# Performance work log

Hardware: AMD Instinct MI355X
Metric: run time of the kernel (lower is better)

Reference implementation:

```python
import jax, jax.numpy as jnp
import numpy as np
from jax import lax

K = 512          # num_embeddings
D = 64           # embedding_dim
BETA = 0.25      # commitment_cost


def _conv(x, w, b, stride, pad):
    y = lax.conv_general_dilated(x, w, (stride, stride), ((pad, pad), (pad, pad)),
                                 dimension_numbers=('NCHW', 'OIHW', 'NCHW'))
    return y + b[None, :, None, None]


def _convT(x, w, b, stride, k, pad):
    # transposed conv as lhs-dilated conv; w is OIHW with O=out_channels
    p = k - 1 - pad
    y = lax.conv_general_dilated(x, w, (1, 1), ((p, p), (p, p)),
                                 lhs_dilation=(stride, stride),
                                 dimension_numbers=('NCHW', 'OIHW', 'NCHW'))
    return y + b[None, :, None, None]


def setup_inputs() -> dict:
    key = jax.random.key(0)
    ks = jax.random.split(key, 16)
    s = 0.05
    inp = {
        'x':   jax.random.uniform(ks[0], (16, 3, 256, 256), jnp.float32),
        'w1':  jax.random.normal(ks[1], (128, 3, 4, 4), jnp.float32) * s,
        'b1':  jnp.zeros((128,), jnp.float32),
        'w2':  jax.random.normal(ks[2], (256, 128, 4, 4), jnp.float32) * s,
        'b2':  jnp.zeros((256,), jnp.float32),
        'w3':  jax.random.normal(ks[3], (D, 256, 3, 3), jnp.float32) * s,
        'b3':  jnp.zeros((D,), jnp.float32),
        'emb': jax.random.uniform(ks[4], (K, D), jnp.float32, -1.0 / K, 1.0 / K),
        'wt1': jax.random.normal(ks[5], (256, D, 4, 4), jnp.float32) * s,
        'bt1': jnp.zeros((256,), jnp.float32),
        'wt2': jax.random.normal(ks[6], (128, 256, 4, 4), jnp.float32) * s,
        'bt2': jnp.zeros((128,), jnp.float32),
        'w4':  jax.random.normal(ks[7], (3, 128, 3, 3), jnp.float32) * s,
        'b4':  jnp.zeros((3,), jnp.float32),
    }
    return inp


def reference(x, w1, b1, w2, b2, w3, b3, emb, wt1, bt1, wt2, bt2, w4, b4):
    # ---- encoder ----
    h = jax.nn.relu(_conv(x, w1, b1, 2, 1))    # [B,128,128,128]
    h = jax.nn.relu(_conv(h, w2, b2, 2, 1))    # [B,256,64,64]
    z = _conv(h, w3, b3, 1, 1)                 # [B,64,64,64]

    # ---- vector quantizer (faithful raw-memory reshape, as in source) ----
    flat_z = z.reshape(-1, D)                                 # [N,D]
    dists = (jnp.sum(flat_z ** 2, axis=1, keepdims=True)
             + jnp.sum(emb ** 2, axis=1)
             - 2.0 * flat_z @ emb.T)                          # [N,K]
    idx = jnp.argmin(dists, axis=1)                           # [N]
    quantized = emb[idx].reshape(z.shape)                     # gather == onehot @ emb

    e_latent = jnp.mean((lax.stop_gradient(quantized) - z) ** 2)
    q_latent = jnp.mean((quantized - lax.stop_gradient(z)) ** 2)
    vq_loss = q_latent + BETA * e_latent

    z_q = z + lax.stop_gradient(quantized - z)                # straight-through

    n = flat_z.shape[0]
    avg_probs = jnp.zeros((K,), jnp.float32).at[idx].add(1.0) / n
    perplexity = jnp.exp(-jnp.sum(avg_probs * jnp.log(avg_probs + 1e-10)))

    # ---- decoder (computed in the original forward; its output is unused) ----
    d = jax.nn.relu(_convT(z_q, wt1, bt1, 2, 4, 1))           # [B,256,128,128]
    d = jax.nn.relu(_convT(d, wt2, bt2, 2, 4, 1))             # [B,128,256,256]
    _x_recon = jax.nn.sigmoid(_conv(d, w4, b4, 1, 1))         # [B,3,256,256]

    return (z_q, vq_loss, perplexity)
```

## Files before the change

### kernel.cpp

```cpp
#include <hip/hip_runtime.h>
#include <math.h>

typedef __attribute__((ext_vector_type(8))) short bf16x8;
typedef __attribute__((ext_vector_type(4))) float f32x4;
typedef __attribute__((ext_vector_type(4))) unsigned u32x4;
typedef __attribute__((ext_vector_type(2))) unsigned u32x2;

#define H1P_OFF  0ull
#define H2P_OFF  35143680ull
#define WQ2H_OFF 53526528ull
#define WQ2L_OFF 53788672ull
#define WQ3H_OFF 54050816ull
#define WQ3L_OFF 54149120ull
#define EQ_OFF   54247424ull
#define EN_OFF   54280192ull
#define HIST_OFF 54280704ull
#define SSEP_OFF 54284800ull
#define WQ1H_OFF 54285824ull
#define WQ1L_OFF 54289920ull

__device__ inline unsigned short f2bf(float f) {
  unsigned u = __builtin_bit_cast(unsigned, f);
  return (unsigned short)((u + 0x7fffu + ((u >> 16) & 1u)) >> 16);
}
__device__ inline float bf2f(unsigned short h) {
  return __builtin_bit_cast(float, (unsigned)h << 16);
}
__device__ inline unsigned packsplit(float v) {
  unsigned short h = f2bf(v);
  unsigned short l = f2bf(v - bf2f(h));
  return (unsigned)h | ((unsigned)l << 16);
}
#define SEL_HI 0x05040100u
#define SEL_LO 0x07060302u
__device__ inline bf16x8 mkfrag(const u32x4 p, const u32x4 q, unsigned sel) {
  u32x4 r;
  r[0] = __builtin_amdgcn_perm(p[1], p[0], sel);
  r[1] = __builtin_amdgcn_perm(p[3], p[2], sel);
  r[2] = __builtin_amdgcn_perm(q[1], q[0], sel);
  r[3] = __builtin_amdgcn_perm(q[3], q[2], sel);
  return __builtin_bit_cast(bf16x8, r);
}

__global__ void pack_wq1_k(const float* __restrict__ w, unsigned short* __restrict__ wh) {
  int i = blockIdx.x * 256 + threadIdx.x;
  if (i >= 8192) return;
  int j = i & 7, l = (i >> 3) & 63, fg = (i >> 9) & 7, ks = i >> 12;
  int row = fg * 16 + (l & 15);
  int k = ks * 32 + (l >> 4) * 8 + j;
  int ci = k >> 4, r = k & 15, kh = r >> 2, kw = r & 3;
  wh[i] = (ci < 3) ? f2bf(w[((row * 3 + ci) * 4 + kh) * 4 + kw]) : (unsigned short)0;
}
__global__ void pack_wq2_k(const float* __restrict__ w, unsigned short* __restrict__ wh) {
  int i = blockIdx.x * 256 + threadIdx.x;
  if (i >= 524288) return;
  int j = i & 7, l = (i >> 3) & 63, fg = (i >> 9) & 15, ks = i >> 13;
  int row = fg * 16 + (l & 15);
  int k = ks * 32 + (l >> 4) * 8 + j;
  wh[i] = f2bf(w[row * 2048 + k]);
}
__global__ void pack_wq3_k(const float* __restrict__ w, unsigned short* __restrict__ wh) {
  int i = blockIdx.x * 256 + threadIdx.x;
  if (i >= 196608) return;
  int j = i & 7, l = (i >> 3) & 63, fg = (i >> 9) & 3, ks = i >> 11;
  int row = fg * 16 + (l & 15);
  int k = ks * 32 + (l >> 4) * 8 + j;
  int ci = k / 12, rb = k - ci * 12, kh = rb >> 2, kw = rb & 3;
  wh[i] = (kw < 3) ? f2bf(w[((row * 256 + ci) * 3 + kh) * 3 + kw]) : (unsigned short)0;
}
__global__ void pack_eq_k(const float* __restrict__ emb, unsigned* __restrict__ eq,
                          float* __restrict__ enorm) {
  int i = blockIdx.x * 256 + threadIdx.x;
  if (i < 32768) {
    int e = i & 3, l = (i >> 2) & 63, j = (i >> 8) & 1, fg = (i >> 9) & 31, ks = i >> 14;
    int row = fg * 16 + (l & 15);
    int d = ks * 32 + (l >> 4) * 8 + j * 4 + e;
    eq[i] = packsplit(emb[row * 64 + d]);
  }
  if (i < 512) {
    float s = 0.f;
#pragma unroll
    for (int d = 0; d < 64; ++d) { float e = emb[i * 64 + d]; s += e * e; }
    enorm[i] = s;
  }
}

__global__ void pack_x1_k(const float* __restrict__ x, unsigned* __restrict__ xp) {
  int i = blockIdx.x * 256 + threadIdx.x;
  if (i >= 16 * 4 * 258 * 260) return;
  int b = i / 268320, r = i - b * 268320;
  int ci = r / 67080, r2 = r - ci * 67080;
  int iy = r2 / 260, ix = r2 - iy * 260;
  unsigned v = 0u;
  if (ci < 3 && iy >= 1 && iy <= 256 && ix >= 1 && ix <= 256)
    v = packsplit(x[((b * 3 + ci) * 256 + (iy - 1)) * 256 + (ix - 1)]);
  xp[i] = v;
}

__global__ void halo_k(unsigned* __restrict__ h1p, unsigned* __restrict__ h2p) {
  int i = blockIdx.x * 256 + threadIdx.x;
  if (i < 2048 * 520) {
    int p = i / 520, c = i - p * 520; int r, cc;
    if (c < 132)      { r = 0;   cc = c; }
    else if (c < 264) { r = 129; cc = c - 132; }
    else if (c < 392) { r = c - 264 + 1; cc = 0; }
    else              { r = c - 392 + 1; cc = 129; }
    h1p[(size_t)p * 130 * 132 + r * 132 + cc] = 0u;
  } else {
    int j = i - 2048 * 520;
    if (j >= 4096 * 328) return;
    int p = j / 328, c = j - p * 328; int r, cc;
    if (c < 68)       { r = 0;  cc = c; }
    else if (c < 136) { r = 65; cc = c - 68; }
    else { int c2 = c - 136; int which = c2 >> 6; r = 1 + (c2 & 63);
           cc = (which == 0) ? 0 : (which == 1 ? 65 : 66); }
    h2p[(size_t)p * 66 * 68 + r * 68 + cc] = 0u;
  }
}

template <int IC, int KHW, int OC, int IHP, int IWP, int S, int NWX, int NWC,
          int YB, bool WIDE, int OSR, int OSP, int OPAD, bool SPLIT_OUT, int D>
__global__ __launch_bounds__(256, 2) void convmm_k(const unsigned* __restrict__ inp,
                                                   const unsigned short* __restrict__ wqh,
                                                   const float* __restrict__ bias,
                                                   unsigned* __restrict__ outp,
                                                   float* __restrict__ outf) {
  constexpr int K = IC * KHW;
  constexpr int KSUPER = K / (32 * D);
  constexpr int FGTOT = OC / 16;
  constexpr int NFRAG = OC / NWC / 16;
  constexpr int MR = 64 * NWX;
  constexpr int CELLS = (MR / 32) * D;
  constexpr int GPLANE = MR * 16;
  constexpr int HBYTES = MR * 64 * D;
  constexpr int ABYTES = MR * 128 * D;
  constexpr int LOG2NWX = (NWX == 2) ? 1 : 0;
  constexpr int LOG2MR = (NWX == 2) ? 7 : 6;

  __shared__ char smem[2 * ABYTES];

  const int tid = threadIdx.x, l = tid & 63, wv = tid >> 6;
  const int orig = (blockIdx.x & 7) * ((int)gridDim.x >> 3) + (blockIdx.x >> 3);
  const int bb = orig >> YB;
  const int y0 = orig & ((1 << YB) - 1);
  const int rsel = l & 15, gp = l >> 4;
  const int mbase = (wv & (NWX - 1)) * 64;
  const int fgbase = (wv >> LOG2NWX) * NFRAG;
  const int nbase = fgbase * 16;

  const int arow = tid & (MR - 1);
  int qs[CELLS];
  const unsigned* abase[CELLS];
#pragma unroll
  for (int c = 0; c < CELLS; ++c) {
    qs[c] = (tid >> LOG2MR) * CELLS + c;
    if constexpr (KHW == 16) {
      int ci0 = qs[c] >> 2, kh = qs[c] & 3;
      abase[c] = inp + (((size_t)bb * IC + ci0) * IHP + (S * y0 + kh)) * IWP + S * arow;
    }
  }

  f32x4 acc[NFRAG][4];
#pragma unroll
  for (int nf = 0; nf < NFRAG; ++nf)
#pragma unroll
    for (int xf = 0; xf < 4; ++xf) acc[nf][xf] = (f32x4){0.f, 0.f, 0.f, 0.f};

  unsigned avA[CELLS][4], avB[CELLS][4];
  bf16x8 brA[D][NFRAG], brB[D][NFRAG];

  auto loadA = [&](int ks, unsigned (&av)[CELLS][4]) {
#pragma unroll
    for (int c = 0; c < CELLS; ++c) {
      if constexpr (KHW == 16) {
        const unsigned* p = abase[c];
        av[c][0] = p[0]; av[c][1] = p[1]; av[c][2] = p[2]; av[c][3] = p[3];
        abase[c] += (size_t)(2 * D) * IHP * IWP;
      } else {
        int k = ks * (32 * D) + qs[c] * 4;
        int ci = (k * 5462) >> 16;
        int rb = k - ci * 12;
        int kh = rb >> 2;
        int yl = arow >> 6, x = arow & 63;
        const unsigned* p = inp + (((size_t)bb * IC + ci) * IHP + (y0 * 2 + yl + kh)) * IWP + x;
        av[c][0] = p[0]; av[c][1] = p[1]; av[c][2] = p[2]; av[c][3] = p[3];
      }
    }
  };
  auto writeA = [&](int buf, unsigned (&av)[CELLS][4]) {
    char* base = smem + buf * ABYTES;
#pragma unroll
    for (int cp = 0; cp < CELLS / 2; ++cp) {
      int q0 = qs[2 * cp];
      int off = (q0 >> 1) * GPLANE + (arow << 4);
      u32x4 h, lo;
      h[0]  = __builtin_amdgcn_perm(av[2 * cp][1],     av[2 * cp][0],     SEL_HI);
      h[1]  = __builtin_amdgcn_perm(av[2 * cp][3],     av[2 * cp][2],     SEL_HI);
      h[2]  = __builtin_amdgcn_perm(av[2 * cp + 1][1], av[2 * cp + 1][0], SEL_HI);
      h[3]  = __builtin_amdgcn_perm(av[2 * cp + 1][3], av[2 * cp + 1][2], SEL_HI);
      lo[0] = __builtin_amdgcn_perm(av[2 * cp][1],     av[2 * cp][0],     SEL_LO);
      lo[1] = __builtin_amdgcn_perm(av[2 * cp][3],     av[2 * cp][2],     SEL_LO);
      lo[2] = __builtin_amdgcn_perm(av[2 * cp + 1][1], av[2 * cp + 1][0], SEL_LO);
      lo[3] = __builtin_amdgcn_perm(av[2 * cp + 1][3], av[2 * cp + 1][2], SEL_LO);
      *(u32x4*)(base + off) = h;
      *(u32x4*)(base + HBYTES + off) = lo;
    }
  };
  auto loadB = [&](int ks, bf16x8 (&bh)[D][NFRAG]) {
#pragma unroll
    for (int s = 0; s < D; ++s)
#pragma unroll
      for (int nf = 0; nf < NFRAG; ++nf) {
        size_t idx = (((size_t)((ks * D + s) * FGTOT + fgbase + nf) * 64) + l) * 8;
        bh[s][nf] = *(const bf16x8*)(wqh + idx);
      }
  };
  auto step = [&](int ks, bf16x8 (&ch)[D][NFRAG], bf16x8 (&nh)[D][NFRAG],
                  unsigned (&avW)[CELLS][4], unsigned (&avL)[CELLS][4]) {
    const bool hasW = (ks + 1 < KSUPER);
    const bool hasL = (ks + 2 < KSUPER);
    if (hasW) loadB(ks + 1, nh);
    if (hasL) loadA(ks + 2, avL);
    const char* bA = smem + (ks & 1) * ABYTES;
#pragma unroll
    for (int s = 0; s < D; ++s) {
      bf16x8 ah[4], al[4];
#pragma unroll
      for (int xf = 0; xf < 4; ++xf) {
        int row = mbase + xf * 16 + rsel;
        ah[xf] = *(const bf16x8*)(bA + (s * 4 + gp) * GPLANE + (row << 4));
        al[xf] = *(const bf16x8*)(bA + HBYTES + (s * 4 + gp) * GPLANE + (row << 4));
      }
#pragma unroll
      for (int nf = 0; nf < NFRAG; ++nf) {
#pragma unroll
        for (int xf = 0; xf < 4; ++xf) {
          acc[nf][xf] = __builtin_amdgcn_mfma_f32_16x16x32_bf16(ch[s][nf], ah[xf], acc[nf][xf], 0, 0, 0);
          acc[nf][xf] = __builtin_amdgcn_mfma_f32_16x16x32_bf16(ch[s][nf], al[xf], acc[nf][xf], 0, 0, 0);
        }
      }
    }
    if (hasW) writeA((ks & 1) ^ 1, avW);
    __syncthreads();
  };

  loadB(0, brA);
  loadA(0, avA);
  writeA(0, avA);
  if (KSUPER > 1) loadA(1, avB);
  __syncthreads();

#pragma unroll 1
  for (int ks = 0; ks < KSUPER; ks += 2) {
    step(ks,     brA, brB, avB, avA);
    step(ks + 1, brB, brA, avA, avB);
  }

#pragma unroll
  for (int nf = 0; nf < NFRAG; ++nf) {
    int n0 = nbase + nf * 16 + (l >> 4) * 4;
#pragma unroll
    for (int xf = 0; xf < 4; ++xf) {
      int m = mbase + xf * 16 + rsel;
      int xo, yout;
      if constexpr (WIDE) { xo = m; yout = y0; }
      else { xo = m & 63; yout = y0 * NWX + (m >> 6); }
#pragma unroll
      for (int r = 0; r < 4; ++r) {
        float v = acc[nf][xf][r] + bias[n0 + r];
        if constexpr (SPLIT_OUT) {
          if (v < 0.f) v = 0.f;
          outp[((size_t)bb * OC + n0 + r) * OSP + (size_t)(yout + OPAD) * OSR + (xo + OPAD)] =
              packsplit(v);
        } else {
          outf[((size_t)bb * OC + n0 + r) * OSP + (size_t)yout * OSR + xo] = v;
        }
      }
    }
  }
}

__global__ __launch_bounds__(256, 2) void vqmm_k(float* __restrict__ zq,
                                                 const float* __restrict__ emb,
                                                 const unsigned* __restrict__ eq,
                                                 const float* __restrict__ enorm,
                                                 unsigned* __restrict__ hist,
                                                 float* __restrict__ ssep) {
  const int tid = threadIdx.x, l = tid & 63, wv = tid >> 6;
  float* zsrc = zq + (size_t)blockIdx.x * 4096;

  __shared__ float zf[64][64];
  __shared__ unsigned zp[4096];
  __shared__ float candd[4][64];
  __shared__ int   candi[4][64];
  __shared__ int   idxf[64];
  __shared__ unsigned hcnt[512];
  __shared__ float wsse[4];

  for (int i = tid; i < 512; i += 256) hcnt[i] = 0;

#pragma unroll
  for (int p = 0; p < 4; ++p) {
    int idx = p * 256 + tid;
    float4 v = *(const float4*)(zsrc + (size_t)idx * 4);
    int n = idx >> 4, d0 = (idx & 15) * 4;
    zf[n][d0 + 0] = v.x; zf[n][d0 + 1] = v.y;
    zf[n][d0 + 2] = v.z; zf[n][d0 + 3] = v.w;
  }
  __syncthreads();
#pragma unroll
  for (int p = 0; p < 16; ++p) {
    int idx = p * 256 + tid;
    int n = idx >> 6, d = idx & 63;
    zp[(n << 6) + ((((d >> 2) ^ (n & 15)) << 2) | (d & 3))] = packsplit(zf[n][d]);
  }
  __syncthreads();

  f32x4 acc[8][4];
#pragma unroll
  for (int nf = 0; nf < 8; ++nf)
#pragma unroll
    for (int xf = 0; xf < 4; ++xf) acc[nf][xf] = (f32x4){0.f, 0.f, 0.f, 0.f};

  const int rsel = l & 15;
#pragma unroll
  for (int ks = 0; ks < 2; ++ks) {
    bf16x8 ah[4], al[4];
    const int gk = ks * 8 + (l >> 4) * 2;
#pragma unroll
    for (int xf = 0; xf < 4; ++xf) {
      int n = xf * 16 + rsel;
      u32x4 p0 = *(const u32x4*)((const char*)zp + (n << 8) + ((gk ^ (n & 15)) << 4));
      u32x4 p1 = *(const u32x4*)((const char*)zp + (n << 8) + (((gk + 1) ^ (n & 15)) << 4));
      ah[xf] = mkfrag(p0, p1, SEL_HI);
      al[xf] = mkfrag(p0, p1, SEL_LO);
    }
#pragma unroll
    for (int nf = 0; nf < 8; ++nf) {
      int fg = wv * 8 + nf;
      u32x4 b0 = *(const u32x4*)(eq + (((size_t)((ks * 32 + fg) * 2 + 0)) << 8) + (l << 2));
      u32x4 b1 = *(const u32x4*)(eq + (((size_t)((ks * 32 + fg) * 2 + 1)) << 8) + (l << 2));
      bf16x8 wh = mkfrag(b0, b1, SEL_HI);
      bf16x8 wl = mkfrag(b0, b1, SEL_LO);
#pragma unroll
      for (int xf = 0; xf < 4; ++xf) {
        acc[nf][xf] = __builtin_amdgcn_mfma_f32_16x16x32_bf16(wh, ah[xf], acc[nf][xf], 0, 0, 0);
        acc[nf][xf] = __builtin_amdgcn_mfma_f32_16x16x32_bf16(wh, al[xf], acc[nf][xf], 0, 0, 0);
        acc[nf][xf] = __builtin_amdgcn_mfma_f32_16x16x32_bf16(wl, ah[xf], acc[nf][xf], 0, 0, 0);
      }
    }
  }

  float en[8][4];
#pragma unroll
  for (int nf = 0; nf < 8; ++nf)
#pragma unroll
    for (int r = 0; r < 4; ++r)
      en[nf][r] = enorm[wv * 128 + nf * 16 + (l >> 4) * 4 + r];

#pragma unroll
  for (int xf = 0; xf < 4; ++xf) {
    float best = 1e30f; int bidx = 0;
#pragma unroll
    for (int nf = 0; nf < 8; ++nf)
#pragma unroll
      for (int r = 0; r < 4; ++r) {
        int k = wv * 128 + nf * 16 + (l >> 4) * 4 + r;
        float dist = en[nf][r] - 2.f * acc[nf][xf][r];
        if (dist < best || (dist == best && k < bidx)) { best = dist; bidx = k; }
      }
#pragma unroll
    for (int off = 16; off <= 32; off <<= 1) {
      float ob = __shfl_xor(best, off, 64);
      int oi = __shfl_xor(bidx, off, 64);
      if (ob < best || (ob == best && oi < bidx)) { best = ob; bidx = oi; }
    }
    if (l < 16) { candd[wv][xf * 16 + l] = best; candi[wv][xf * 16 + l] = bidx; }
  }
  __syncthreads();
  if (tid < 64) {
    float best = candd[0][tid]; int bidx = candi[0][tid];
#pragma unroll
    for (int w = 1; w < 4; ++w) {
      float ob = candd[w][tid]; int oi = candi[w][tid];
      if (ob < best || (ob == best && oi < bidx)) { best = ob; bidx = oi; }
    }
    idxf[tid] = bidx;
    atomicAdd(&hcnt[bidx], 1u);
  }
  __syncthreads();

  float sse = 0.f;
#pragma unroll
  for (int p = 0; p < 16; ++p) {
    int idx = p * 256 + tid;
    int n = idx >> 6, d = idx & 63;
    float q = emb[idxf[n] * 64 + d];
    float z = zf[n][d];
    float df = q - z;
    sse += df * df;
    zsrc[idx] = q;
  }
#pragma unroll
  for (int off = 32; off > 0; off >>= 1) sse += __shfl_down(sse, off, 64);
  if (l == 0) wsse[wv] = sse;

  unsigned* hr = hist + ((blockIdx.x & 7) << 9);
  __syncthreads();
  for (int i = tid; i < 512; i += 256)
    if (hcnt[i]) atomicAdd(&hr[i], hcnt[i]);
  if (tid == 0) ssep[blockIdx.x] = wsse[0] + wsse[1] + wsse[2] + wsse[3];
}

__global__ void fin_k(const unsigned* __restrict__ hist,
                      const float* __restrict__ ssep,
                      float* __restrict__ out) {
  __shared__ float red[512];
  __shared__ float sred[512];
  int t = threadIdx.x;
  sred[t] = ssep[t] + ssep[t + 512];
  unsigned c = 0;
#pragma unroll
  for (int r = 0; r < 8; ++r) c += hist[(r << 9) + t];
  float p = (float)c * (1.f / 65536.f);
  red[t] = p * logf(p + 1e-10f);
  __syncthreads();
  for (int s = 256; s > 0; s >>= 1) {
    if (t < s) { red[t] += red[t + s]; sred[t] += sred[t + s]; }
    __syncthreads();
  }
  if (t == 0) {
    out[4194304] = 1.25f * sred[0] * (1.f / 4194304.f);
    out[4194305] = expf(-red[0]);
  }
}

extern "C" void kernel_launch(void* const* d_in, const int* in_sizes, int n_in,
                              void* d_out, int out_size, void* d_ws, size_t ws_size,
                              hipStream_t stream) {
  const float* x   = (const float*)d_in[0];
  const float* w1  = (const float*)d_in[1];
  const float* b1  = (const float*)d_in[2];
  const float* w2  = (const float*)d_in[3];
  const float* b2  = (const float*)d_in[4];
  const float* w3  = (const float*)d_in[5];
  const float* b3  = (const float*)d_in[6];
  const float* emb = (const float*)d_in[7];

  float* out = (float*)d_out;
  unsigned* wsu = (unsigned*)d_ws;
  unsigned* h1p = wsu + H1P_OFF;
  unsigned* h2p = wsu + H2P_OFF;
  unsigned* x1p = wsu + H2P_OFF;
  unsigned short* wq1h = (unsigned short*)(wsu + WQ1H_OFF);
  unsigned short* wq2h = (unsigned short*)(wsu + WQ2H_OFF);
  unsigned short* wq3h = (unsigned short*)(wsu + WQ3H_OFF);
  unsigned* eqp = wsu + EQ_OFF;
  float* enorm = (float*)(wsu + EN_OFF);
  unsigned* hist = wsu + HIST_OFF;
  float* ssep = (float*)(wsu + SSEP_OFF);

  hipMemsetAsync(wsu + HIST_OFF, 0, 4096 * sizeof(unsigned), stream);

  pack_wq1_k<<<dim3(32),   dim3(256), 0, stream>>>(w1, wq1h);
  pack_wq2_k<<<dim3(2048), dim3(256), 0, stream>>>(w2, wq2h);
  pack_wq3_k<<<dim3(768),  dim3(256), 0, stream>>>(w3, wq3h);
  pack_eq_k<<<dim3(128),   dim3(256), 0, stream>>>(emb, eqp, enorm);
  pack_x1_k<<<dim3(16770), dim3(256), 0, stream>>>(x, x1p);

  convmm_k<4, 16, 128, 258, 260, 2, 2, 2, 7, true, 132, 17160, 1, true, 1>
      <<<dim3(2048), dim3(256), 0, stream>>>(x1p, wq1h, b1, h1p, nullptr);
  halo_k<<<dim3(9408), dim3(256), 0, stream>>>(h1p, h2p);
  convmm_k<128, 16, 256, 130, 132, 2, 1, 4, 6, false, 68, 4488, 1, true, 2>
      <<<dim3(1024), dim3(256), 0, stream>>>(h1p, wq2h, b2, h2p, nullptr);
  convmm_k<256, 12, 64, 66, 68, 1, 2, 2, 5, false, 64, 4096, 0, false, 2>
      <<<dim3(512), dim3(256), 0, stream>>>(h2p, wq3h, b3, nullptr, out);

  vqmm_k<<<dim3(1024), dim3(256), 0, stream>>>(out, emb, eqp, enorm, hist, ssep);
  fin_k<<<dim3(1), dim3(512), 0, stream>>>(hist, ssep, out);
}
```

Measured before the change: 292.7 us.

## Fuse input packing into first conv and merge weight pack kernels

Removes the separate pack_x1_k pass that wrote a padded, hi/lo-split copy of the input image. The first conv now reads fp32 x directly, applies the padding bounds check and does the bf16 split in its loader. It also merges the four weight/codebook packing kernels into one launch dispatched by block range. This cuts a large intermediate write/read and several launches, at the cost of uncoalesced-ish per-element loads and more ALU work in conv1's load path.

```diff
diff --git a/kernel.cpp b/kernel.cpp
--- a/kernel.cpp
+++ b/kernel.cpp
@@ -9,15 +9,12 @@
 #define H1P_OFF  0ull
 #define H2P_OFF  35143680ull
 #define WQ2H_OFF 53526528ull
-#define WQ2L_OFF 53788672ull
 #define WQ3H_OFF 54050816ull
-#define WQ3L_OFF 54149120ull
 #define EQ_OFF   54247424ull
 #define EN_OFF   54280192ull
 #define HIST_OFF 54280704ull
 #define SSEP_OFF 54284800ull
 #define WQ1H_OFF 54285824ull
-#define WQ1L_OFF 54289920ull
 
 __device__ inline unsigned short f2bf(float f) {
   unsigned u = __builtin_bit_cast(unsigned, f);
@@ -42,59 +39,47 @@
   return __builtin_bit_cast(bf16x8, r);
 }
 
-__global__ void pack_wq1_k(const float* __restrict__ w, unsigned short* __restrict__ wh) {
-  int i = blockIdx.x * 256 + threadIdx.x;
-  if (i >= 8192) return;
-  int j = i & 7, l = (i >> 3) & 63, fg = (i >> 9) & 7, ks = i >> 12;
-  int row = fg * 16 + (l & 15);
-  int k = ks * 32 + (l >> 4) * 8 + j;
-  int ci = k >> 4, r = k & 15, kh = r >> 2, kw = r & 3;
-  wh[i] = (ci < 3) ? f2bf(w[((row * 3 + ci) * 4 + kh) * 4 + kw]) : (unsigned short)0;
-}
-__global__ void pack_wq2_k(const float* __restrict__ w, unsigned short* __restrict__ wh) {
-  int i = blockIdx.x * 256 + threadIdx.x;
-  if (i >= 524288) return;
-  int j = i & 7, l = (i >> 3) & 63, fg = (i >> 9) & 15, ks = i >> 13;
-  int row = fg * 16 + (l & 15);
-  int k = ks * 32 + (l >> 4) * 8 + j;
-  wh[i] = f2bf(w[row * 2048 + k]);
-}
-__global__ void pack_wq3_k(const float* __restrict__ w, unsigned short* __restrict__ wh) {
-  int i = blockIdx.x * 256 + threadIdx.x;
-  if (i >= 196608) return;
-  int j = i & 7, l = (i >> 3) & 63, fg = (i >> 9) & 3, ks = i >> 11;
-  int row = fg * 16 + (l & 15);
-  int k = ks * 32 + (l >> 4) * 8 + j;
-  int ci = k / 12, rb = k - ci * 12, kh = rb >> 2, kw = rb & 3;
-  wh[i] = (kw < 3) ? f2bf(w[((row * 256 + ci) * 3 + kh) * 3 + kw]) : (unsigned short)0;
-}
-__global__ void pack_eq_k(const float* __restrict__ emb, unsigned* __restrict__ eq,
-                          float* __restrict__ enorm) {
-  int i = blockIdx.x * 256 + threadIdx.x;
-  if (i < 32768) {
-    int e = i & 3, l = (i >> 2) & 63, j = (i >> 8) & 1, fg = (i >> 9) & 31, ks = i >> 14;
+__global__ void pack_all_k(const float* __restrict__ w1, const float* __restrict__ w2,
+                           const float* __restrict__ w3, const float* __restrict__ emb,
+                           unsigned short* __restrict__ wh1, unsigned short* __restrict__ wh2,
+                           unsigned short* __restrict__ wh3, unsigned* __restrict__ eq,
+                           float* __restrict__ enorm) {
+  int blk = blockIdx.x;
+  if (blk < 2048) {
+    int i = blk * 256 + threadIdx.x;
+    int j = i & 7, l = (i >> 3) & 63, fg = (i >> 9) & 15, ks = i >> 13;
     int row = fg * 16 + (l & 15);
-    int d = ks * 32 + (l >> 4) * 8 + j * 4 + e;
-    eq[i] = packsplit(emb[row * 64 + d]);
-  }
-  if (i < 512) {
-    float s = 0.f;
-#pragma unroll
-    for (int d = 0; d < 64; ++d) { float e = emb[i * 64 + d]; s += e * e; }
-    enorm[i] = s;
-  }
-}
-
-__global__ void pack_x1_k(const float* __restrict__ x, unsigned* __restrict__ xp) {
-  int i = blockIdx.x * 256 + threadIdx.x;
-  if (i >= 16 * 4 * 258 * 260) return;
-  int b = i / 268320, r = i - b * 268320;
-  int ci = r / 67080, r2 = r - ci * 67080;
-  int iy = r2 / 260, ix = r2 - iy * 260;
-  unsigned v = 0u;
-  if (ci < 3 && iy >= 1 && iy <= 256 && ix >= 1 && ix <= 256)
-    v = packsplit(x[((b * 3 + ci) * 256 + (iy - 1)) * 256 + (ix - 1)]);
-  xp[i] = v;
+    int k = ks * 32 + (l >> 4) * 8 + j;
+    wh2[i] = f2bf(w2[row * 2048 + k]);
+  } else if (blk < 2816) {
+    int i = (blk - 2048) * 256 + threadIdx.x;
+    int j = i & 7, l = (i >> 3) & 63, fg = (i >> 9) & 3, ks = i >> 11;
+    int row = fg * 16 + (l & 15);
+    int k = ks * 32 + (l >> 4) * 8 + j;
+    int ci = k / 12, rb = k - ci * 12, kh = rb >> 2, kw = rb & 3;
+    wh3[i] = (kw < 3) ? f2bf(w3[((row * 256 + ci) * 3 + kh) * 3 + kw]) : (unsigned short)0;
+  } else if (blk < 2848) {
+    int i = (blk - 2816) * 256 + threadIdx.x;
+    int j = i & 7, l = (i >> 3) & 63, fg = (i >> 9) & 7, ks = i >> 12;
+    int row = fg * 16 + (l & 15);
+    int k = ks * 32 + (l >> 4) * 8 + j;
+    int ci = k >> 4, r = k & 15, kh = r >> 2, kw = r & 3;
+    wh1[i] = (ci < 3) ? f2bf(w1[((row * 3 + ci) * 4 + kh) * 4 + kw]) : (unsigned short)0;
+  } else {
+    int i = (blk - 2848) * 256 + threadIdx.x;
+    if (i < 32768) {
+      int e = i & 3, l = (i >> 2) & 63, j = (i >> 8) & 1, fg = (i >> 9) & 31, ks = i >> 14;
+      int row = fg * 16 + (l & 15);
+      int d = ks * 32 + (l >> 4) * 8 + j * 4 + e;
+      eq[i] = packsplit(emb[row * 64 + d]);
+    }
+    if (i < 512) {
+      float s = 0.f;
+#pragma unroll
+      for (int d = 0; d < 64; ++d) { float e = emb[i * 64 + d]; s += e * e; }
+      enorm[i] = s;
+    }
+  }
 }
 
 __global__ void halo_k(unsigned* __restrict__ h1p, unsigned* __restrict__ h2p) {
@@ -119,8 +104,9 @@
 }
 
 template <int IC, int KHW, int OC, int IHP, int IWP, int S, int NWX, int NWC,
-          int YB, bool WIDE, int OSR, int OSP, int OPAD, bool SPLIT_OUT, int D>
+          int YB, bool WIDE, int OSR, int OSP, int OPAD, bool SPLIT_OUT, int D, bool XSRC>
 __global__ __launch_bounds__(256, 2) void convmm_k(const unsigned* __restrict__ inp,
+                                                   const float* __restrict__ xsrc,
                                                    const unsigned short* __restrict__ wqh,
                                                    const float* __restrict__ bias,
                                                    unsigned* __restrict__ outp,
@@ -154,7 +140,7 @@
 #pragma unroll
   for (int c = 0; c < CELLS; ++c) {
     qs[c] = (tid >> LOG2MR) * CELLS + c;
-    if constexpr (KHW == 16) {
+    if constexpr (KHW == 16 && !XSRC) {
       int ci0 = qs[c] >> 2, kh = qs[c] & 3;
       abase[c] = inp + (((size_t)bb * IC + ci0) * IHP + (S * y0 + kh)) * IWP + S * arow;
     }
@@ -172,7 +158,18 @@
   auto loadA = [&](int ks, unsigned (&av)[CELLS][4]) {
 #pragma unroll
     for (int c = 0; c < CELLS; ++c) {
-      if constexpr (KHW == 16) {
+      if constexpr (XSRC) {
+        int ci = (qs[c] >> 2) + 2 * D * ks;
+        int kh = qs[c] & 3;
+        int iy = S * y0 + kh - 1;
+        bool yok = (ci < 3) && ((unsigned)iy < 256u);
+        const float* xp = xsrc + ((size_t)(bb * 3 + ci) * 256 + iy) * 256;
+#pragma unroll
+        for (int e = 0; e < 4; ++e) {
+          int ix = S * arow + e - 1;
+          av[c][e] = (yok && (unsigned)ix < 256u) ? packsplit(xp[ix]) : 0u;
+        }
+      } else if constexpr (KHW == 16) {
         const unsigned* p = abase[c];
         av[c][0] = p[0]; av[c][1] = p[1]; av[c][2] = p[2]; av[c][3] = p[3];
         abase[c] += (size_t)(2 * D) * IHP * IWP;
@@ -451,7 +448,6 @@
   unsigned* wsu = (unsigned*)d_ws;
   unsigned* h1p = wsu + H1P_OFF;
   unsigned* h2p = wsu + H2P_OFF;
-  unsigned* x1p = wsu + H2P_OFF;
   unsigned short* wq1h = (unsigned short*)(wsu + WQ1H_OFF);
   unsigned short* wq2h = (unsigned short*)(wsu + WQ2H_OFF);
   unsigned short* wq3h = (unsigned short*)(wsu + WQ3H_OFF);
@@ -462,19 +458,16 @@
 
   hipMemsetAsync(wsu + HIST_OFF, 0, 4096 * sizeof(unsigned), stream);
 
-  pack_wq1_k<<<dim3(32),   dim3(256), 0, stream>>>(w1, wq1h);
-  pack_wq2_k<<<dim3(2048), dim3(256), 0, stream>>>(w2, wq2h);
-  pack_wq3_k<<<dim3(768),  dim3(256), 0, stream>>>(w3, wq3h);
-  pack_eq_k<<<dim3(128),   dim3(256), 0, stream>>>(emb, eqp, enorm);
-  pack_x1_k<<<dim3(16770), dim3(256), 0, stream>>>(x, x1p);
-
-  convmm_k<4, 16, 128, 258, 260, 2, 2, 2, 7, true, 132, 17160, 1, true, 1>
-      <<<dim3(2048), dim3(256), 0, stream>>>(x1p, wq1h, b1, h1p, nullptr);
+  pack_all_k<<<dim3(2976), dim3(256), 0, stream>>>(w1, w2, w3, emb,
+                                                   wq1h, wq2h, wq3h, eqp, enorm);
   halo_k<<<dim3(9408), dim3(256), 0, stream>>>(h1p, h2p);
-  convmm_k<128, 16, 256, 130, 132, 2, 1, 4, 6, false, 68, 4488, 1, true, 2>
-      <<<dim3(1024), dim3(256), 0, stream>>>(h1p, wq2h, b2, h2p, nullptr);
-  convmm_k<256, 12, 64, 66, 68, 1, 2, 2, 5, false, 64, 4096, 0, false, 2>
-      <<<dim3(512), dim3(256), 0, stream>>>(h2p, wq3h, b3, nullptr, out);
+
+  convmm_k<4, 16, 128, 258, 260, 2, 2, 2, 7, true, 132, 17160, 1, true, 1, true>
+      <<<dim3(2048), dim3(256), 0, stream>>>(nullptr, x, wq1h, b1, h1p, nullptr);
+  convmm_k<128, 16, 256, 130, 132, 2, 1, 4, 6, false, 68, 4488, 1, true, 2, false>
+      <<<dim3(1024), dim3(256), 0, stream>>>(h1p, nullptr, wq2h, b2, h2p, nullptr);
+  convmm_k<256, 12, 64, 66, 68, 1, 2, 2, 5, false, 64, 4096, 0, false, 2, false>
+      <<<dim3(512), dim3(256), 0, stream>>>(h2p, nullptr, wq3h, b3, nullptr, out);
 
   vqmm_k<<<dim3(1024), dim3(256), 0, stream>>>(out, emb, eqp, enorm, hist, ssep);
   fin_k<<<dim3(1), dim3(512), 0, stream>>>(hist, ssep, out);
```

Result: no change. 289.2 us (median of 2 runs) (-1.2%).
